# Optimization experiments

Measured on AMD Instinct MI355X. Metric: run time of the kernel, lower is better.

Reference implementation:

```python
import jax, jax.numpy as jnp
import numpy as np

K = 8            # hard-attention top-k neighbors per node
NEG_SLOPE = 0.2  # leaky relu slope


def setup_inputs() -> dict:
    key = jax.random.key(0)
    k1, k2, k3, k4, k5, k6 = jax.random.split(key, 6)
    N, D, F = 50000, 64, 256
    H, O = 8, 32
    feat = jax.random.normal(k1, (N, F), dtype=jnp.float32)
    neighbors = jax.random.randint(k2, (N, D), 0, N)  # src node ids per dst
    # learned params (xavier-normal-ish scale)
    p = jax.random.normal(k3, (1, F), dtype=jnp.float32) * float(np.sqrt(2.0 / (1 + F)))
    W = jax.random.normal(k4, (F, H * O), dtype=jnp.float32) * float(np.sqrt(2.0 / (F + H * O)))
    attn_l = jax.random.normal(k5, (1, H, O), dtype=jnp.float32) * float(np.sqrt(2.0 / (H * O + 1)))
    attn_r = jax.random.normal(k6, (1, H, O), dtype=jnp.float32) * float(np.sqrt(2.0 / (H * O + 1)))
    return {"feat": feat, "neighbors": neighbors, "p": p, "W": W,
            "attn_l": attn_l, "attn_r": attn_r}


def reference(feat, neighbors, p, W, attn_l, attn_r):
    N, F = feat.shape
    H, O = attn_l.shape[1], attn_l.shape[2]
    # node projection score y = |p . x| / ||p||
    y = jnp.abs(feat @ p[0]) / jnp.linalg.norm(p)          # [N]
    # hard top-k neighbor selection by source score (select_topk on 'y')
    ys = y[neighbors]                                       # [N, D]
    _, idx = jax.lax.top_k(ys, K)                           # [N, K]
    src = jnp.take_along_axis(neighbors, idx, axis=1)       # [N, K] source ids
    # gating + projection
    gate = jax.nn.sigmoid(y) * 2.0                          # [N]
    ft = ((gate[:, None] * feat) @ W).reshape(N, H, O)      # [N, H, O]
    el = jnp.sum(ft * attn_l, axis=-1)                      # [N, H]
    er = jnp.sum(ft * attn_r, axis=-1)                      # [N, H]
    # edge scores: u_add_v, leaky_relu, edge_softmax over each dst's K edges
    e = el[src] + er[:, None, :]                            # [N, K, H]
    e = jnp.where(e > 0, e, NEG_SLOPE * e)
    a = jax.nn.softmax(e, axis=1)                           # [N, K, H]
    # u_mul_e + sum aggregation
    rst = jnp.einsum('nkh,nkho->nho', a, ft[src])           # [N, H, O]
    return jax.nn.elu(rst)
```

## Files before the change

### kernel.cpp

```cpp
#include <hip/hip_runtime.h>
#include <math.h>

#define NEG_SLOPE 0.2f

typedef _Float16 half8 __attribute__((ext_vector_type(8)));
typedef _Float16 half2v __attribute__((ext_vector_type(2)));
typedef float floatx4 __attribute__((ext_vector_type(4)));

__device__ __forceinline__ float dot4f(float4 a, float4 b) {
    return a.x * b.x + a.y * b.y + a.z * b.z + a.w * b.w;
}

static __device__ __forceinline__ unsigned short f2h(float x) {
    _Float16 h = (_Float16)x;
    return __builtin_bit_cast(unsigned short, h);
}

__global__ void k_prepw(const float* __restrict__ W,
                        const float* __restrict__ al,
                        const float* __restrict__ ar,
                        unsigned short* __restrict__ Wtp,
                        unsigned short* __restrict__ Mp) {
    const int k = threadIdx.x;
    if (blockIdx.x < 256) {
        const int c = blockIdx.x;
        float v = W[(size_t)k * 256 + c];
        Wtp[(size_t)(c >> 4) * 4096 + (k >> 3) * 128 + (c & 15) * 8 + (k & 7)] = f2h(v);
    } else {
        const int t = blockIdx.x - 256;
        float v = 0.f;
        if (t < 8) {
            if ((k >> 5) == t) v = al[t * 32 + (k & 31)];
        } else {
            if ((k >> 5) == (t - 8)) v = ar[(t - 8) * 32 + (k & 31)];
        }
        Mp[(k >> 3) * 128 + t * 8 + (k & 7)] = f2h(v);
    }
}

__global__ __launch_bounds__(256) void k_fused(const float4* __restrict__ feat4,
                                               const float4* __restrict__ p4,
                                               const unsigned short* __restrict__ Wtp,
                                               const unsigned short* __restrict__ Mp,
                                               float* __restrict__ y,
                                               unsigned short* __restrict__ fth,
                                               float* __restrict__ el,
                                               float* __restrict__ er,
                                               int N) {
    __shared__ unsigned short As[32][264];
    __shared__ float Gs[32];
    const int lane = threadIdx.x & 63;
    const int w = threadIdx.x >> 6;
    const int l16 = lane & 15, quad = lane >> 4;
    const int nb = blockIdx.x * 32;

    const float4 p = p4[lane];

    float dp[8];
#pragma unroll
    for (int j = 0; j < 8; ++j) {
        const int m = w * 8 + j;
        int n = nb + m;
        if (n >= N) n = N - 1;
        float4 f = feat4[(size_t)n * 64 + lane];
        dp[j] = dot4f(f, p);
        ushort4 u;
        u.x = f2h(f.x);
        u.y = f2h(f.y);
        u.z = f2h(f.z);
        u.w = f2h(f.w);
        *(ushort4*)&As[m][lane * 4] = u;
    }
    __syncthreads();

    floatx4 acc[2][4];
#pragma unroll
    for (int mt = 0; mt < 2; ++mt)
#pragma unroll
        for (int ct = 0; ct < 4; ++ct) acc[mt][ct] = (floatx4){0.f, 0.f, 0.f, 0.f};

    const unsigned short* bbase = Wtp + (size_t)(w * 4) * 4096 + quad * 128 + l16 * 8;

#define KSTEP(ks)                                                                     \
    {                                                                                 \
        half8 a0 = *(const half8*)&As[l16][(ks) + quad * 8];                          \
        half8 a1 = *(const half8*)&As[16 + l16][(ks) + quad * 8];                     \
        const unsigned short* bk = bbase + ((ks) >> 3) * 128;                         \
        half8 b0 = *(const half8*)(bk);                                               \
        half8 b1 = *(const half8*)(bk + 4096);                                        \
        half8 b2 = *(const half8*)(bk + 8192);                                        \
        half8 b3 = *(const half8*)(bk + 12288);                                       \
        acc[0][0] = __builtin_amdgcn_mfma_f32_16x16x32_f16(a0, b0, acc[0][0], 0, 0, 0); \
        acc[0][1] = __builtin_amdgcn_mfma_f32_16x16x32_f16(a0, b1, acc[0][1], 0, 0, 0); \
        acc[0][2] = __builtin_amdgcn_mfma_f32_16x16x32_f16(a0, b2, acc[0][2], 0, 0, 0); \
        acc[0][3] = __builtin_amdgcn_mfma_f32_16x16x32_f16(a0, b3, acc[0][3], 0, 0, 0); \
        acc[1][0] = __builtin_amdgcn_mfma_f32_16x16x32_f16(a1, b0, acc[1][0], 0, 0, 0); \
        acc[1][1] = __builtin_amdgcn_mfma_f32_16x16x32_f16(a1, b1, acc[1][1], 0, 0, 0); \
        acc[1][2] = __builtin_amdgcn_mfma_f32_16x16x32_f16(a1, b2, acc[1][2], 0, 0, 0); \
        acc[1][3] = __builtin_amdgcn_mfma_f32_16x16x32_f16(a1, b3, acc[1][3], 0, 0, 0); \
    }

    KSTEP(0)
    KSTEP(32)
    KSTEP(64)
    KSTEP(96)

    {
        float pp = dot4f(p, p);
#pragma unroll
        for (int off = 32; off; off >>= 1) pp += __shfl_xor(pp, off, 64);
        const float rnorm = 1.0f / sqrtf(pp);
#pragma unroll
        for (int j = 0; j < 8; ++j) {
            float d = dp[j];
#pragma unroll
            for (int off = 32; off; off >>= 1) d += __shfl_xor(d, off, 64);
            float yv = fabsf(d) * rnorm;
            const int m = w * 8 + j;
            const int n = nb + m;
            if (lane == 0) {
                if (n < N) y[n] = yv;
                Gs[m] = 2.0f / (1.0f + __expf(-yv));
            }
        }
    }

    KSTEP(128)
    KSTEP(160)
    KSTEP(192)
    KSTEP(224)
#undef KSTEP

    __syncthreads();
#pragma unroll
    for (int mt = 0; mt < 2; ++mt)
#pragma unroll
        for (int ct = 0; ct < 4; ++ct)
#pragma unroll
            for (int i = 0; i < 4; ++i) {
                int row = mt * 16 + quad * 4 + i;
                int col = w * 64 + ct * 16 + l16;
                unsigned short hv = f2h(Gs[row] * acc[mt][ct][i]);
                As[row][col] = hv;
                int grow = nb + row;
                if (grow < N) fth[(size_t)grow * 256 + col] = hv;
            }
    __syncthreads();

    if (w < 2) {
        floatx4 d = (floatx4){0.f, 0.f, 0.f, 0.f};
        for (int ks = 0; ks < 256; ks += 32) {
            half8 a = *(const half8*)&As[w * 16 + l16][ks + quad * 8];
            half8 b = *(const half8*)(Mp + (ks >> 3) * 128 + quad * 128 + l16 * 8);
            d = __builtin_amdgcn_mfma_f32_16x16x32_f16(a, b, d, 0, 0, 0);
        }
#pragma unroll
        for (int i = 0; i < 4; ++i) {
            int row = nb + w * 16 + quad * 4 + i;
            if (row < N) {
                if (l16 < 8) el[(size_t)row * 8 + l16] = d[i];
                else         er[(size_t)row * 8 + (l16 - 8)] = d[i];
            }
        }
    }
}

__global__ __launch_bounds__(256) void k_aggr(const int* __restrict__ nbr,
                                              const float* __restrict__ y,
                                              const uint2* __restrict__ fth2,
                                              const float* __restrict__ el,
                                              const float* __restrict__ er,
                                              floatx4* __restrict__ out4,
                                              int N) {
    const int lane = threadIdx.x & 63;
    const int n = blockIdx.x * 4 + (threadIdx.x >> 6);
    if (n >= N) return;
    const int h = lane >> 3;

    const int s = nbr[(size_t)n * 64 + lane];
    const unsigned int key = __float_as_uint(y[s]);

    unsigned long long selmask = 0ull;
    unsigned int t = 0u;
#pragma unroll 1
    for (int b = 30; b >= 0; --b) {
        unsigned int cand = t | (1u << b);
        unsigned long long m = __ballot(key >= cand);
        int c = __popcll(m);
        if (c >= 8) {
            t = cand;
            if (c == 8) { selmask = m; break; }
        }
    }
    if (selmask == 0ull) {
        const unsigned long long gtmask = __ballot(key > t);
        const int ngt = __popcll(gtmask);
        const unsigned long long eqmask = __ballot(key == t);
        const unsigned long long below = (1ull << lane) - 1ull;
        const int eqrank = __popcll(eqmask & below);
        const bool in8 = (key > t) | ((key == t) & (eqrank < 8 - ngt));
        selmask = __ballot(in8);
    }

    int srck[8];
#pragma unroll
    for (int k = 0; k < 8; ++k) {
        int l = __ffsll((long long)selmask) - 1;
        srck[k] = __builtin_amdgcn_readlane(s, l);
        selmask &= selmask - 1ull;
    }

    uint2 vk[8];
#pragma unroll
    for (int k = 0; k < 8; ++k) vk[k] = fth2[(size_t)srck[k] * 64 + lane];

    const float erv = er[(size_t)n * 8 + h];
    float e[8];
#pragma unroll
    for (int k = 0; k < 8; ++k) {
        float ev = el[(size_t)srck[k] * 8 + h] + erv;
        e[k] = ev > 0.f ? ev : NEG_SLOPE * ev;
    }

    float m01 = fmaxf(e[0], e[1]), m23 = fmaxf(e[2], e[3]);
    float m45 = fmaxf(e[4], e[5]), m67 = fmaxf(e[6], e[7]);
    float m = fmaxf(fmaxf(m01, m23), fmaxf(m45, m67));
    float sum = 0.f;
#pragma unroll
    for (int k = 0; k < 8; ++k) {
        e[k] = __expf(e[k] - m);
        sum += e[k];
    }
    const float inv = 1.0f / sum;

    half2v acc0 = (half2v){(_Float16)0, (_Float16)0};
    half2v acc1 = acc0;
#pragma unroll
    for (int k = 0; k < 8; ++k) {
        _Float16 ah = (_Float16)(e[k] * inv);
        half2v a2 = {ah, ah};
        acc0 += a2 * __builtin_bit_cast(half2v, vk[k].x);
        acc1 += a2 * __builtin_bit_cast(half2v, vk[k].y);
    }
    floatx4 r;
    r[0] = (float)acc0[0];
    r[1] = (float)acc0[1];
    r[2] = (float)acc1[0];
    r[3] = (float)acc1[1];
    r[0] = r[0] > 0.f ? r[0] : __expf(r[0]) - 1.f;
    r[1] = r[1] > 0.f ? r[1] : __expf(r[1]) - 1.f;
    r[2] = r[2] > 0.f ? r[2] : __expf(r[2]) - 1.f;
    r[3] = r[3] > 0.f ? r[3] : __expf(r[3]) - 1.f;
    __builtin_nontemporal_store(r, &out4[(size_t)n * 64 + lane]);
}

extern "C" void kernel_launch(void* const* d_in, const int* in_sizes, int n_in,
                              void* d_out, int out_size, void* d_ws, size_t ws_size,
                              hipStream_t stream) {
    const float* feat = (const float*)d_in[0];
    const int* nbr    = (const int*)d_in[1];
    const float* p    = (const float*)d_in[2];
    const float* W    = (const float*)d_in[3];
    const float* al   = (const float*)d_in[4];
    const float* ar   = (const float*)d_in[5];

    const int N = in_sizes[0] / 256;

    float* y = (float*)d_ws;
    unsigned short* Wtp = (unsigned short*)(y + N);
    unsigned short* Mp  = Wtp + 256 * 256;
    float* el = (float*)(Mp + 32 * 128);
    float* er = el + (size_t)N * 8;
    unsigned short* fth = (unsigned short*)(er + (size_t)N * 8);

    k_prepw<<<272, 256, 0, stream>>>(W, al, ar, Wtp, Mp);
    k_fused<<<(N + 31) / 32, 256, 0, stream>>>((const float4*)feat, (const float4*)p,
                                               Wtp, Mp, y, fth, el, er, N);
    k_aggr<<<(N + 3) / 4, 256, 0, stream>>>(nbr, y, (const uint2*)fth, el, er,
                                            (floatx4*)d_out, N);
}
```

Measured before the change: 170.6 us.

## Restructure aggregation lanes: per-lane softmax via shuffles and 16-byte neighbor row gathers

The softmax now gives each lane one (neighbor, head) pair, so a single el load per lane replaces eight, and max and sum are reduced with cross-lane shuffles. The feature gather splits the wave into two halves that each load whole 512-byte fp16 rows with 16-byte loads, four loads per lane instead of eight 8-byte loads. The two halves' partial sums are combined with an xor-32 shuffle, and the output index is remapped to match. This cuts the count of memory instructions and redundant el loads in exchange for extra shuffles and select logic.

New measurement: 175.3 us. +2.7%, slower.

```diff
diff --git a/kernel.cpp b/kernel.cpp
--- a/kernel.cpp
+++ b/kernel.cpp
@@ -167,7 +167,7 @@
 
 __global__ __launch_bounds__(256) void k_aggr(const int* __restrict__ nbr,
                                               const float* __restrict__ y,
-                                              const uint2* __restrict__ fth2,
+                                              const unsigned short* __restrict__ fth,
                                               const float* __restrict__ el,
                                               const float* __restrict__ er,
                                               floatx4* __restrict__ out4,
@@ -175,7 +175,6 @@
     const int lane = threadIdx.x & 63;
     const int n = blockIdx.x * 4 + (threadIdx.x >> 6);
     if (n >= N) return;
-    const int h = lane >> 3;
 
     const int s = nbr[(size_t)n * 64 + lane];
     const unsigned int key = __float_as_uint(y[s]);
@@ -210,48 +209,66 @@
         selmask &= selmask - 1ull;
     }
 
-    uint2 vk[8];
-#pragma unroll
-    for (int k = 0; k < 8; ++k) vk[k] = fth2[(size_t)srck[k] * 64 + lane];
-
-    const float erv = er[(size_t)n * 8 + h];
-    float e[8];
-#pragma unroll
-    for (int k = 0; k < 8; ++k) {
-        float ev = el[(size_t)srck[k] * 8 + h] + erv;
-        e[k] = ev > 0.f ? ev : NEG_SLOPE * ev;
-    }
-
-    float m01 = fmaxf(e[0], e[1]), m23 = fmaxf(e[2], e[3]);
-    float m45 = fmaxf(e[4], e[5]), m67 = fmaxf(e[6], e[7]);
-    float m = fmaxf(fmaxf(m01, m23), fmaxf(m45, m67));
-    float sum = 0.f;
-#pragma unroll
-    for (int k = 0; k < 8; ++k) {
-        e[k] = __expf(e[k] - m);
-        sum += e[k];
-    }
-    const float inv = 1.0f / sum;
+    const int j = lane >> 3;
+    int s01 = (j & 1) ? srck[1] : srck[0];
+    int s23 = (j & 1) ? srck[3] : srck[2];
+    int s45 = (j & 1) ? srck[5] : srck[4];
+    int s67 = (j & 1) ? srck[7] : srck[6];
+    int s03 = (j & 2) ? s23 : s01;
+    int s47 = (j & 2) ? s67 : s45;
+    int sj  = (j & 4) ? s47 : s03;
+    const float elv = el[(size_t)sj * 8 + (lane & 7)];
+    const float erv = er[(size_t)n * 8 + (lane & 7)];
+    float e = elv + erv;
+    e = e > 0.f ? e : NEG_SLOPE * e;
+
+    float mx = e;
+    mx = fmaxf(mx, __shfl_xor(mx, 8, 64));
+    mx = fmaxf(mx, __shfl_xor(mx, 16, 64));
+    mx = fmaxf(mx, __shfl_xor(mx, 32, 64));
+    float ex = __expf(e - mx);
+    float sum = ex;
+    sum += __shfl_xor(sum, 8, 64);
+    sum += __shfl_xor(sum, 16, 64);
+    sum += __shfl_xor(sum, 32, 64);
+    const float av = ex * (1.0f / sum);
+
+    const int m31 = lane & 31;
+    const int half = lane >> 5;
+    const int hcol = m31 >> 2;
+    const int wbase = half * 8 + hcol;
 
     half2v acc0 = (half2v){(_Float16)0, (_Float16)0};
-    half2v acc1 = acc0;
-#pragma unroll
-    for (int k = 0; k < 8; ++k) {
-        _Float16 ah = (_Float16)(e[k] * inv);
+    half2v acc1 = acc0, acc2 = acc0, acc3 = acc0;
+#pragma unroll
+    for (int tt = 0; tt < 4; ++tt) {
+        int rt = half ? srck[2 * tt + 1] : srck[2 * tt];
+        uint4 v = *(const uint4*)&fth[(size_t)rt * 256 + m31 * 8];
+        float af = __shfl(av, 16 * tt + wbase, 64);
+        _Float16 ah = (_Float16)af;
         half2v a2 = {ah, ah};
-        acc0 += a2 * __builtin_bit_cast(half2v, vk[k].x);
-        acc1 += a2 * __builtin_bit_cast(half2v, vk[k].y);
-    }
+        acc0 += a2 * __builtin_bit_cast(half2v, v.x);
+        acc1 += a2 * __builtin_bit_cast(half2v, v.y);
+        acc2 += a2 * __builtin_bit_cast(half2v, v.z);
+        acc3 += a2 * __builtin_bit_cast(half2v, v.w);
+    }
+    acc0 += __builtin_bit_cast(half2v, __shfl_xor(__builtin_bit_cast(int, acc0), 32, 64));
+    acc1 += __builtin_bit_cast(half2v, __shfl_xor(__builtin_bit_cast(int, acc1), 32, 64));
+    acc2 += __builtin_bit_cast(half2v, __shfl_xor(__builtin_bit_cast(int, acc2), 32, 64));
+    acc3 += __builtin_bit_cast(half2v, __shfl_xor(__builtin_bit_cast(int, acc3), 32, 64));
+
+    half2v lo = half ? acc2 : acc0;
+    half2v hi = half ? acc3 : acc1;
     floatx4 r;
-    r[0] = (float)acc0[0];
-    r[1] = (float)acc0[1];
-    r[2] = (float)acc1[0];
-    r[3] = (float)acc1[1];
+    r[0] = (float)lo[0];
+    r[1] = (float)lo[1];
+    r[2] = (float)hi[0];
+    r[3] = (float)hi[1];
     r[0] = r[0] > 0.f ? r[0] : __expf(r[0]) - 1.f;
     r[1] = r[1] > 0.f ? r[1] : __expf(r[1]) - 1.f;
     r[2] = r[2] > 0.f ? r[2] : __expf(r[2]) - 1.f;
     r[3] = r[3] > 0.f ? r[3] : __expf(r[3]) - 1.f;
-    __builtin_nontemporal_store(r, &out4[(size_t)n * 64 + lane]);
+    __builtin_nontemporal_store(r, &out4[(size_t)n * 64 + 2 * m31 + half]);
 }
 
 extern "C" void kernel_launch(void* const* d_in, const int* in_sizes, int n_in,
@@ -276,6 +293,6 @@
     k_prepw<<<272, 256, 0, stream>>>(W, al, ar, Wtp, Mp);
     k_fused<<<(N + 31) / 32, 256, 0, stream>>>((const float4*)feat, (const float4*)p,
                                                Wtp, Mp, y, fth, el, er, N);
-    k_aggr<<<(N + 3) / 4, 256, 0, stream>>>(nbr, y, (const uint2*)fth, el, er,
+    k_aggr<<<(N + 3) / 4, 256, 0, stream>>>(nbr, y, fth, el, er,
                                             (floatx4*)d_out, N);
 }
```
